# Performance work log

Hardware: AMD Instinct MI355X
Metric: run time of the kernel (lower is better)

## Reference

```python
import jax, jax.numpy as jnp
import numpy as np

B, LQ, LK, D, H, DK, DV = 8, 1024, 1024, 512, 8, 64, 64
EPS = 1e-14          # K.epsilon()**2 with default K.epsilon()=1e-7
MASK_VALUE = -1e30   # default mask_value in call()


def setup_inputs() -> dict:
    key = jax.random.key(0)
    ks = jax.random.split(key, 7)
    query = jax.random.normal(ks[0], (B, LQ, D), jnp.float32)
    key_t = jax.random.normal(ks[1], (B, LK, D), jnp.float32)
    value = jax.random.normal(ks[2], (B, LK, D), jnp.float32)
    mask = jax.random.randint(ks[3], (B, LK), 0, 2).astype(jnp.float32)
    glorot = np.sqrt(2.0 / (D + DK)).astype(np.float32)
    Wq = jax.random.normal(ks[4], (H, D, DK), jnp.float32) * glorot
    Wk = jax.random.normal(ks[5], (H, D, DK), jnp.float32) * glorot
    Wv = jax.random.normal(ks[6], (H, D, DV), jnp.float32) * glorot
    gamma = jnp.ones((1,), jnp.float32)
    beta = jnp.zeros((1,), jnp.float32)
    return {"query": query, "key": key_t, "value": value, "mask": mask,
            "Wq": Wq, "Wk": Wk, "Wv": Wv, "gamma": gamma, "beta": beta}


def reference(query, key, value, mask, Wq, Wk, Wv, gamma, beta):
    # Per-head projections (the original's Python loop over heads, vectorized).
    q = jnp.einsum('bqd,hde->bhqe', query, Wq)   # [B,H,LQ,DK]
    k = jnp.einsum('bkd,hde->bhke', key, Wk)     # [B,H,LK,DK]
    v = jnp.einsum('bkd,hde->bhke', value, Wv)   # [B,H,LK,DV]
    # NOTE: no 1/sqrt(dk) scaling, faithful to the source.
    A = jnp.einsum('bhqe,bhke->bhqk', q, k)      # [B,H,LQ,LK]
    m = mask[:, None, None, :]                    # [B,1,1,LK] broadcast over heads & queries
    A = m * A + (1.0 - m) * MASK_VALUE
    A = jax.nn.softmax(A, axis=-1)
    o = jnp.einsum('bhqk,bhke->bhqe', A, v)      # [B,H,LQ,DV]
    conc = o.transpose(0, 2, 1, 3).reshape(B, LQ, H * DV)  # concat heads
    # Scalar-affine layernorm over the concatenated feature dim.
    mean = jnp.mean(conc, axis=-1, keepdims=True)
    var = jnp.mean(jnp.square(conc - mean), axis=-1, keepdims=True)
    x = (conc - mean) / jnp.sqrt(var + EPS)
    return x * gamma[0] + beta[0]
```

## Files before the change

### kernel.cpp

```cpp
#include <hip/hip_runtime.h>
#include <math.h>

#define NB 8
#define NLQ 1024
#define NLK 1024
#define ND 512
#define NH 8
#define MASKV -1e30f
#define LOG2E 1.44269504088896f
#define SHIFT2 32.0f

typedef unsigned short ushort_t;
typedef __attribute__((ext_vector_type(8))) _Float16 f16x8;
typedef __attribute__((ext_vector_type(8))) short bf16x8;
typedef __attribute__((ext_vector_type(16))) float f32x16;

__device__ __forceinline__ ushort_t f2h_bits(float f) {
    union { _Float16 h; ushort_t u; } v; v.h = (_Float16)f;
    return v.u;
}
__device__ __forceinline__ ushort_t f2bf(float f) {
    union { float f; unsigned u; } v; v.f = f;
    unsigned r = v.u + 0x7fffu + ((v.u >> 16) & 1u);
    return (ushort_t)(r >> 16);
}
__device__ __forceinline__ void gload16(const ushort_t* g, ushort_t* l) {
    __builtin_amdgcn_global_load_lds(
        (const __attribute__((address_space(1))) void*)g,
        (__attribute__((address_space(3))) void*)l, 16, 0, 0);
}
__device__ __forceinline__ unsigned pack_bf16_trunc(float p0, float p1) {
    return __builtin_amdgcn_perm(__float_as_uint(p1), __float_as_uint(p0),
                                 0x07060302u);
}
__device__ __forceinline__ unsigned pack_f16(float a, float b) {
    return (unsigned)f2h_bits(a) | ((unsigned)f2h_bits(b) << 16);
}
__device__ __forceinline__ unsigned pack_bf16_rne(float a, float b) {
    return (unsigned)f2bf(a) | ((unsigned)f2bf(b) << 16);
}

__global__ __launch_bounds__(256) void wsplit_kernel(
    const float* __restrict__ Wq, const float* __restrict__ Wk, const float* __restrict__ Wv,
    ushort_t* __restrict__ oq, ushort_t* __restrict__ ok, ushort_t* __restrict__ ov) {
    __shared__ float T[64][65];
    const int d0 = blockIdx.x * 64;
    const int h  = blockIdx.y;
    const int t  = blockIdx.z;
    const float* W = (t == 0) ? Wq : (t == 1) ? Wk : Wv;
    ushort_t* oh = (t == 0) ? oq : (t == 1) ? ok : ov;
    const float scale = (t == 0) ? LOG2E : 1.f;
    const int tid = threadIdx.x;
#pragma unroll
    for (int i = 0; i < 4; i++) {
        int r = (tid >> 4) + i * 16;
        int c = (tid & 15) * 4;
        float4 v = *(const float4*)&W[((size_t)h * ND + d0 + r) * 64 + c];
        *(float4*)&T[r][c] = v;
    }
    __syncthreads();
    const int e = tid & 63;
    const int dg = tid >> 6;
    ushort_t hs[16];
#pragma unroll
    for (int dd = 0; dd < 16; dd++) hs[dd] = f2h_bits(T[dg * 16 + dd][e] * scale);
    size_t base = ((size_t)h * 64 + e) * ND + d0 + dg * 16;
#pragma unroll
    for (int c = 0; c < 2; c++) {
        uint4 wh;
        wh.x = (unsigned)hs[8*c+0] | ((unsigned)hs[8*c+1] << 16);
        wh.y = (unsigned)hs[8*c+2] | ((unsigned)hs[8*c+3] << 16);
        wh.z = (unsigned)hs[8*c+4] | ((unsigned)hs[8*c+5] << 16);
        wh.w = (unsigned)hs[8*c+6] | ((unsigned)hs[8*c+7] << 16);
        *(uint4*)&oh[base + 8 * c] = wh;
    }
}

__global__ __launch_bounds__(256, 3) void proj_mfma_kernel(
    const float* __restrict__ Xq, const float* __restrict__ Xk,
    const float* __restrict__ Xv, const ushort_t* __restrict__ Wbase,
    ushort_t* __restrict__ Obase) {
    __shared__ ushort_t sX[2][16 * 520];
    __shared__ ushort_t sW[2][8 * 520];

    const int lb = blockIdx.x * 128;
    const int h  = blockIdx.y;
    const int z  = blockIdx.z;
    const int t  = z >> 3;
    const int b  = z & 7;
    const int tid  = threadIdx.x;
    const int wave = tid >> 6;
    const int lane = tid & 63;
    const int l31  = lane & 31;
    const int hib  = lane >> 5;
    const int lhalf = wave & 1;
    const int ehalf = wave >> 1;
    const size_t bh = (size_t)b * NH + h;

    const float* Xt = (t == 0) ? Xq : (t == 1) ? Xk : Xv;
    const float* gx = Xt + ((size_t)b * NLQ + lb) * ND;
    const ushort_t* gw = Wbase + (size_t)t * ((size_t)NH * 64 * ND)
                       + (size_t)h * 64 * ND;
    ushort_t* out = Obase + (size_t)t * ((size_t)NB * NH * NLQ * 64);

    const int srow = lane >> 3;
    const int schk = (lane & 7) ^ srow;
    const int dslot = srow * 64 + (lane & 7) * 8;

    auto stage_w = [&](int buf, int d0) {
#pragma unroll
        for (int i = 0; i < 2; i++) {
            int u = i * 4 + wave;
            int row = u * 8 + srow;
            gload16(gw + (size_t)row * ND + d0 + schk * 8, sW[buf] + u * 520);
        }
    };
    auto load_x = [&](int d0, float4* xa, float4* xb) {
#pragma unroll
        for (int i = 0; i < 4; i++) {
            int u = i * 4 + wave;
            int row = u * 8 + srow;
            const float* src = gx + (size_t)row * ND + d0 + schk * 8;
            xa[i] = *(const float4*)src;
            xb[i] = *(const float4*)(src + 4);
        }
    };
    auto write_x = [&](int buf, const float4* xa, const float4* xb) {
#pragma unroll
        for (int i = 0; i < 4; i++) {
            int u = i * 4 + wave;
            uint4 w;
            w.x = pack_f16(xa[i].x, xa[i].y);
            w.y = pack_f16(xa[i].z, xa[i].w);
            w.z = pack_f16(xb[i].x, xb[i].y);
            w.w = pack_f16(xb[i].z, xb[i].w);
            *(uint4*)&sX[buf][u * 520 + dslot] = w;
        }
    };

    f32x16 acc0, acc1;
#pragma unroll
    for (int i = 0; i < 16; i++) { acc0[i] = 0.f; acc1[i] = 0.f; }

    const int arow0 = lhalf * 64 + l31;
    const int apad0 = (arow0 >> 3) * 520 + (arow0 & 7) * 64;
    const int apad1 = apad0 + 4 * 520;
    const int brow  = ehalf * 32 + l31;
    const int bpad  = (brow >> 3) * 520 + (brow & 7) * 64;
    const int sw = l31 & 7;

    {
        float4 xa[4], xb[4];
        load_x(0, xa, xb);
        stage_w(0, 0);
        write_x(0, xa, xb);
    }
    __syncthreads();
    int cur = 0;
    for (int kc = 0; kc < 8; kc++) {
        float4 xa[4], xb[4];
        if (kc < 7) {
            load_x((kc + 1) * 64, xa, xb);
            stage_w(cur ^ 1, (kc + 1) * 64);
        }
#pragma unroll
        for (int c = 0; c < 4; c++) {
            const int pc = ((2 * c + hib) ^ sw) * 8;
            f16x8 a0 = *(const f16x8*)&sX[cur][apad0 + pc];
            f16x8 a1 = *(const f16x8*)&sX[cur][apad1 + pc];
            f16x8 wv = *(const f16x8*)&sW[cur][bpad + pc];
            acc0 = __builtin_amdgcn_mfma_f32_32x32x16_f16(a0, wv, acc0, 0, 0, 0);
            acc1 = __builtin_amdgcn_mfma_f32_32x32x16_f16(a1, wv, acc1, 0, 0, 0);
        }
        if (kc < 7) write_x(cur ^ 1, xa, xb);
        __syncthreads();
        cur ^= 1;
    }

    if (t < 2) {
        const size_t ob = (bh * NLQ + lb + lhalf * 64) * 64;
        const int e = ehalf * 32 + l31;
#pragma unroll
        for (int r = 0; r < 16; r++) {
            int lr = (r & 3) + 8 * (r >> 2) + 4 * hib;
            out[ob + (size_t)lr * 64 + e]        = f2h_bits(acc0[r]);
            out[ob + (size_t)(32 + lr) * 64 + e] = f2h_bits(acc1[r]);
        }
    } else {
        ushort_t (*T)[136] = (ushort_t(*)[136])sX;
        const int e = ehalf * 32 + l31;
#pragma unroll
        for (int g = 0; g < 4; g++) {
            int lr = lhalf * 64 + 8 * g + 4 * hib;
            uint2 w0, w1;
            w0.x = pack_bf16_rne(acc0[4 * g + 0], acc0[4 * g + 1]);
            w0.y = pack_bf16_rne(acc0[4 * g + 2], acc0[4 * g + 3]);
            w1.x = pack_bf16_rne(acc1[4 * g + 0], acc1[4 * g + 1]);
            w1.y = pack_bf16_rne(acc1[4 * g + 2], acc1[4 * g + 3]);
            *(uint2*)&T[e][lr]      = w0;
            *(uint2*)&T[e][lr + 32] = w1;
        }
        __syncthreads();
        const int e2 = tid >> 2;
        const int lc = (tid & 3) * 32;
        size_t basev = (bh * 64 + e2) * NLK + lb + lc;
#pragma unroll
        for (int c4 = 0; c4 < 4; c4++)
            *(uint4*)&out[basev + c4 * 8] = *(const uint4*)&T[e2][lc + c4 * 8];
    }
}

__global__ __launch_bounds__(256, 4) void attn_kernel(
    const ushort_t* __restrict__ Qf, const ushort_t* __restrict__ Kf,
    const ushort_t* __restrict__ Vt, const float* __restrict__ maskp,
    float* __restrict__ Op) {
    __shared__ ushort_t sK[2][4160];
    __shared__ ushort_t sV[2][4160];
    __shared__ float sBias[1024];

    const int idx = blockIdx.x;
    const int bh_i = idx & 63;
    const int qc  = idx >> 6;
    const int b = bh_i >> 3, h = bh_i & 7;
    const size_t bh = (size_t)b * NH + h;

    const int tid  = threadIdx.x;
    const int wave = tid >> 6;
    const int lane = tid & 63;
    const int l31  = lane & 31;
    const int hib  = lane >> 5;
    const int q = qc * 128 + wave * 32 + l31;
    const int sw = l31 & 7;

    {
        const float* mrow = maskp + ((size_t)b << 10);
        float4 m0 = *(const float4*)&mrow[tid * 4];
        float4 bi;
        bi.x = (m0.x > 0.5f) ? -SHIFT2 : MASKV;
        bi.y = (m0.y > 0.5f) ? -SHIFT2 : MASKV;
        bi.z = (m0.z > 0.5f) ? -SHIFT2 : MASKV;
        bi.w = (m0.w > 0.5f) ? -SHIFT2 : MASKV;
        *(float4*)&sBias[tid * 4] = bi;
    }

    f16x8 qh[4];
    {
        const ushort_t* ph = Qf + (bh * NLQ + q) * 64 + hib * 8;
#pragma unroll
        for (int c = 0; c < 4; c++) qh[c] = *(const f16x8*)(ph + c * 16);
    }

    const int srow = lane >> 3;
    const int schk = (lane & 7) ^ srow;

    auto stage = [&](int buf, int k0) {
#pragma unroll
        for (int n = 0; n < 4; n++) {
            int u = wave + n * 4;
            if (u < 8) {
                int row = u * 8 + srow;
                int key = (row & ~12) | ((row & 4) << 1) | ((row & 8) >> 1);
                gload16(Kf + ((bh << 10) + k0 + key) * 64 + schk * 8,
                        sK[buf] + u * 520);
            } else {
                int u8 = u - 8;
                int row = u8 * 8 + srow;
                gload16(Vt + ((bh << 6) + row) * NLK + k0 + schk * 8,
                        sV[buf] + u8 * 520);
            }
        }
    };

    f32x16 O0, O1;
#pragma unroll
    for (int i = 0; i < 16; i++) { O0[i] = 0.f; O1[i] = 0.f; }
    float lrun = 0.f;

    const int rp0 = (l31 >> 3) * 520 + (l31 & 7) * 64;
    const int rp1 = rp0 + 4 * 520;

    stage(0, 0);
    __syncthreads();
    int cur = 0;

    for (int t = 0; t < 16; t++) {
        const int k0 = t << 6;
        if (t < 15) stage(cur ^ 1, k0 + 64);

        f32x16 S0, S1;
#pragma unroll
        for (int g = 0; g < 4; g++) {
            const int kb = k0 + 16 * (g >> 1) + 8 * hib + 4 * (g & 1);
            float4 b0 = *(const float4*)&sBias[kb];
            float4 b1 = *(const float4*)&sBias[kb + 32];
            S0[4 * g + 0] = b0.x; S0[4 * g + 1] = b0.y;
            S0[4 * g + 2] = b0.z; S0[4 * g + 3] = b0.w;
            S1[4 * g + 0] = b1.x; S1[4 * g + 1] = b1.y;
            S1[4 * g + 2] = b1.z; S1[4 * g + 3] = b1.w;
        }
#pragma unroll
        for (int c = 0; c < 4; c++) {
            const int pc = ((2 * c + hib) ^ sw) * 8;
            f16x8 a0 = *(const f16x8*)&sK[cur][rp0 + pc];
            f16x8 a1 = *(const f16x8*)&sK[cur][rp1 + pc];
            S0 = __builtin_amdgcn_mfma_f32_32x32x16_f16(a0, qh[c], S0, 0, 0, 0);
            S1 = __builtin_amdgcn_mfma_f32_32x32x16_f16(a1, qh[c], S1, 0, 0, 0);
        }

        unsigned pq[8][2];
#pragma unroll
        for (int g = 0; g < 8; g++) {
            float p0, p1, p2, p3;
            if (g < 4) {
                p0 = __builtin_amdgcn_exp2f(S0[4*g+0]);
                p1 = __builtin_amdgcn_exp2f(S0[4*g+1]);
                p2 = __builtin_amdgcn_exp2f(S0[4*g+2]);
                p3 = __builtin_amdgcn_exp2f(S0[4*g+3]);
            } else {
                p0 = __builtin_amdgcn_exp2f(S1[4*(g-4)+0]);
                p1 = __builtin_amdgcn_exp2f(S1[4*(g-4)+1]);
                p2 = __builtin_amdgcn_exp2f(S1[4*(g-4)+2]);
                p3 = __builtin_amdgcn_exp2f(S1[4*(g-4)+3]);
            }
            lrun += (p0 + p1) + (p2 + p3);
            pq[g][0] = pack_bf16_trunc(p0, p1);
            pq[g][1] = pack_bf16_trunc(p2, p3);
        }

#pragma unroll
        for (int c = 0; c < 4; c++) {
            union { unsigned u[4]; bf16x8 v; } pf;
            pf.u[0] = pq[2 * c][0];     pf.u[1] = pq[2 * c][1];
            pf.u[2] = pq[2 * c + 1][0]; pf.u[3] = pq[2 * c + 1][1];
            const int pc = ((2 * c + hib) ^ sw) * 8;
            bf16x8 v0 = *(const bf16x8*)&sV[cur][rp0 + pc];
            bf16x8 v1 = *(const bf16x8*)&sV[cur][rp1 + pc];
            O0 = __builtin_amdgcn_mfma_f32_32x32x16_bf16(v0, pf.v, O0, 0, 0, 0);
            O1 = __builtin_amdgcn_mfma_f32_32x32x16_bf16(v1, pf.v, O1, 0, 0, 0);
        }
        __syncthreads();
        cur ^= 1;
    }

    lrun += __shfl_xor(lrun, 32);
    const float linv = 1.f / lrun;
    float* obase = Op + ((size_t)(b * NLQ + q)) * (NH * 64) + h * 64;
#pragma unroll
    for (int me = 0; me < 2; me++) {
#pragma unroll
        for (int g = 0; g < 4; g++) {
            int e0 = me * 32 + 8 * g + 4 * hib;
            float4 o;
            if (me == 0) {
                o.x = O0[4 * g + 0] * linv; o.y = O0[4 * g + 1] * linv;
                o.z = O0[4 * g + 2] * linv; o.w = O0[4 * g + 3] * linv;
            } else {
                o.x = O1[4 * g + 0] * linv; o.y = O1[4 * g + 1] * linv;
                o.z = O1[4 * g + 2] * linv; o.w = O1[4 * g + 3] * linv;
            }
            *(float4*)&obase[e0] = o;
        }
    }
}

__global__ __launch_bounds__(256) void ln_kernel(const float* __restrict__ X,
                                                 const float* __restrict__ gamma,
                                                 const float* __restrict__ beta,
                                                 float* __restrict__ out) {
    const int row = blockIdx.x * 4 + (threadIdx.x >> 6);
    const int lane = threadIdx.x & 63;
    const float* x = &X[(size_t)row * 512];
    float4 v0 = *(const float4*)&x[lane * 8];
    float4 v1 = *(const float4*)&x[lane * 8 + 4];
    float sum = v0.x + v0.y + v0.z + v0.w + v1.x + v1.y + v1.z + v1.w;
    float sq = v0.x * v0.x + v0.y * v0.y + v0.z * v0.z + v0.w * v0.w
             + v1.x * v1.x + v1.y * v1.y + v1.z * v1.z + v1.w * v1.w;
#pragma unroll
    for (int off = 32; off > 0; off >>= 1) {
        sum += __shfl_down(sum, off);
        sq  += __shfl_down(sq, off);
    }
    sum = __shfl(sum, 0);
    sq  = __shfl(sq, 0);
    const float mean = sum * (1.f / 512.f);
    const float var = sq * (1.f / 512.f) - mean * mean;
    const float rstd = rsqrtf(var + 1e-14f);
    const float g = gamma[0], be = beta[0];
    float* o = &out[(size_t)row * 512];
    float4 r0, r1;
    r0.x = (v0.x - mean) * rstd * g + be;  r0.y = (v0.y - mean) * rstd * g + be;
    r0.z = (v0.z - mean) * rstd * g + be;  r0.w = (v0.w - mean) * rstd * g + be;
    r1.x = (v1.x - mean) * rstd * g + be;  r1.y = (v1.y - mean) * rstd * g + be;
    r1.z = (v1.z - mean) * rstd * g + be;  r1.w = (v1.w - mean) * rstd * g + be;
    *(float4*)&o[lane * 8] = r0;
    *(float4*)&o[lane * 8 + 4] = r1;
}

extern "C" void kernel_launch(void* const* d_in, const int* in_sizes, int n_in,
                              void* d_out, int out_size, void* d_ws, size_t ws_size,
                              hipStream_t stream) {
    const float* query = (const float*)d_in[0];
    const float* key_t = (const float*)d_in[1];
    const float* value = (const float*)d_in[2];
    const float* mask  = (const float*)d_in[3];
    const float* Wq    = (const float*)d_in[4];
    const float* Wk    = (const float*)d_in[5];
    const float* Wv    = (const float*)d_in[6];
    const float* gamma = (const float*)d_in[7];
    const float* beta  = (const float*)d_in[8];
    float* out = (float*)d_out;

    const size_t A = (size_t)NB * NLQ * ND;
    const size_t WS = (size_t)NH * 64 * ND;
    ushort_t* Qf = (ushort_t*)d_ws;
    ushort_t* Kf = Qf + A;
    ushort_t* Vt = Qf + 2 * A;
    ushort_t* Wt = Qf + 3 * A;

    wsplit_kernel<<<dim3(ND / 64, NH, 3), 256, 0, stream>>>(
        Wq, Wk, Wv, Wt, Wt + WS, Wt + 2 * WS);

    proj_mfma_kernel<<<dim3(NLQ / 128, NH, 24), 256, 0, stream>>>(
        query, key_t, value, Wt, Qf);

    attn_kernel<<<512, 256, 0, stream>>>(Qf, Kf, Vt, mask, out);

    ln_kernel<<<(NB * NLQ) / 4, 256, 0, stream>>>(out, gamma, beta, out);
}
```

Before: 171.1 us.

## Restructure projection kernel: full weight tile resident, per-wave 64-row X pipelines

```diff
diff --git a/kernel.cpp b/kernel.cpp
--- a/kernel.cpp
+++ b/kernel.cpp
@@ -76,14 +76,14 @@
     }
 }
 
-__global__ __launch_bounds__(256, 3) void proj_mfma_kernel(
+__global__ __launch_bounds__(256) void proj_mfma_kernel(
     const float* __restrict__ Xq, const float* __restrict__ Xk,
     const float* __restrict__ Xv, const ushort_t* __restrict__ Wbase,
     ushort_t* __restrict__ Obase) {
-    __shared__ ushort_t sX[2][16 * 520];
-    __shared__ ushort_t sW[2][8 * 520];
-
-    const int lb = blockIdx.x * 128;
+    __shared__ ushort_t sW[8][4160];
+    __shared__ ushort_t sX[4][2][4160];
+
+    const int lb = blockIdx.x * 256;
     const int h  = blockIdx.y;
     const int z  = blockIdx.z;
     const int t  = z >> 3;
@@ -93,12 +93,10 @@
     const int lane = tid & 63;
     const int l31  = lane & 31;
     const int hib  = lane >> 5;
-    const int lhalf = wave & 1;
-    const int ehalf = wave >> 1;
     const size_t bh = (size_t)b * NH + h;
 
     const float* Xt = (t == 0) ? Xq : (t == 1) ? Xk : Xv;
-    const float* gx = Xt + ((size_t)b * NLQ + lb) * ND;
+    const float* gx = Xt + ((size_t)b * NLQ + lb + wave * 64) * ND;
     const ushort_t* gw = Wbase + (size_t)t * ((size_t)NH * 64 * ND)
                        + (size_t)h * 64 * ND;
     ushort_t* out = Obase + (size_t)t * ((size_t)NB * NH * NLQ * 64);
@@ -107,106 +105,116 @@
     const int schk = (lane & 7) ^ srow;
     const int dslot = srow * 64 + (lane & 7) * 8;
 
-    auto stage_w = [&](int buf, int d0) {
+#pragma unroll
+    for (int kc = 0; kc < 8; kc++) {
 #pragma unroll
         for (int i = 0; i < 2; i++) {
             int u = i * 4 + wave;
             int row = u * 8 + srow;
-            gload16(gw + (size_t)row * ND + d0 + schk * 8, sW[buf] + u * 520);
-        }
-    };
-    auto load_x = [&](int d0, float4* xa, float4* xb) {
-#pragma unroll
-        for (int i = 0; i < 4; i++) {
-            int u = i * 4 + wave;
-            int row = u * 8 + srow;
-            const float* src = gx + (size_t)row * ND + d0 + schk * 8;
-            xa[i] = *(const float4*)src;
-            xb[i] = *(const float4*)(src + 4);
-        }
-    };
-    auto write_x = [&](int buf, const float4* xa, const float4* xb) {
-#pragma unroll
-        for (int i = 0; i < 4; i++) {
-            int u = i * 4 + wave;
-            uint4 w;
-            w.x = pack_f16(xa[i].x, xa[i].y);
-            w.y = pack_f16(xa[i].z, xa[i].w);
-            w.z = pack_f16(xb[i].x, xb[i].y);
-            w.w = pack_f16(xb[i].z, xb[i].w);
-            *(uint4*)&sX[buf][u * 520 + dslot] = w;
-        }
-    };
-
-    f32x16 acc0, acc1;
-#pragma unroll
-    for (int i = 0; i < 16; i++) { acc0[i] = 0.f; acc1[i] = 0.f; }
-
-    const int arow0 = lhalf * 64 + l31;
-    const int apad0 = (arow0 >> 3) * 520 + (arow0 & 7) * 64;
+            gload16(gw + (size_t)row * ND + kc * 64 + schk * 8,
+                    sW[kc] + u * 520);
+        }
+    }
+    float4 xa[8], xb[8];
+#pragma unroll
+    for (int g = 0; g < 8; g++) {
+        const float* src = gx + (size_t)(g * 8 + srow) * ND + schk * 8;
+        xa[g] = *(const float4*)src;
+        xb[g] = *(const float4*)(src + 4);
+    }
+    __syncthreads();
+#pragma unroll
+    for (int g = 0; g < 8; g++) {
+        uint4 w;
+        w.x = pack_f16(xa[g].x, xa[g].y);
+        w.y = pack_f16(xa[g].z, xa[g].w);
+        w.z = pack_f16(xb[g].x, xb[g].y);
+        w.w = pack_f16(xb[g].z, xb[g].w);
+        *(uint4*)&sX[wave][0][g * 520 + dslot] = w;
+    }
+
+    f32x16 a00, a01, a10, a11;
+#pragma unroll
+    for (int i = 0; i < 16; i++) { a00[i] = 0.f; a01[i] = 0.f; a10[i] = 0.f; a11[i] = 0.f; }
+
+    const int sw = l31 & 7;
+    const int apad0 = (l31 >> 3) * 520 + (l31 & 7) * 64;
     const int apad1 = apad0 + 4 * 520;
-    const int brow  = ehalf * 32 + l31;
-    const int bpad  = (brow >> 3) * 520 + (brow & 7) * 64;
-    const int sw = l31 & 7;
-
-    {
-        float4 xa[4], xb[4];
-        load_x(0, xa, xb);
-        stage_w(0, 0);
-        write_x(0, xa, xb);
-    }
-    __syncthreads();
+    const int bpad0 = apad0;
+    const int bpad1 = apad1;
+
     int cur = 0;
+#pragma unroll
     for (int kc = 0; kc < 8; kc++) {
-        float4 xa[4], xb[4];
+        float4 ya[8], yb[8];
         if (kc < 7) {
-            load_x((kc + 1) * 64, xa, xb);
-            stage_w(cur ^ 1, (kc + 1) * 64);
+            const float* gsrc = gx + (kc + 1) * 64;
+#pragma unroll
+            for (int g = 0; g < 8; g++) {
+                const float* src = gsrc + (size_t)(g * 8 + srow) * ND + schk * 8;
+                ya[g] = *(const float4*)src;
+                yb[g] = *(const float4*)(src + 4);
+            }
         }
 #pragma unroll
         for (int c = 0; c < 4; c++) {
             const int pc = ((2 * c + hib) ^ sw) * 8;
-            f16x8 a0 = *(const f16x8*)&sX[cur][apad0 + pc];
-            f16x8 a1 = *(const f16x8*)&sX[cur][apad1 + pc];
-            f16x8 wv = *(const f16x8*)&sW[cur][bpad + pc];
-            acc0 = __builtin_amdgcn_mfma_f32_32x32x16_f16(a0, wv, acc0, 0, 0, 0);
-            acc1 = __builtin_amdgcn_mfma_f32_32x32x16_f16(a1, wv, acc1, 0, 0, 0);
-        }
-        if (kc < 7) write_x(cur ^ 1, xa, xb);
-        __syncthreads();
+            f16x8 xv0 = *(const f16x8*)&sX[wave][cur][apad0 + pc];
+            f16x8 xv1 = *(const f16x8*)&sX[wave][cur][apad1 + pc];
+            f16x8 wv0 = *(const f16x8*)&sW[kc][bpad0 + pc];
+            f16x8 wv1 = *(const f16x8*)&sW[kc][bpad1 + pc];
+            a00 = __builtin_amdgcn_mfma_f32_32x32x16_f16(xv0, wv0, a00, 0, 0, 0);
+            a01 = __builtin_amdgcn_mfma_f32_32x32x16_f16(xv0, wv1, a01, 0, 0, 0);
+            a10 = __builtin_amdgcn_mfma_f32_32x32x16_f16(xv1, wv0, a10, 0, 0, 0);
+            a11 = __builtin_amdgcn_mfma_f32_32x32x16_f16(xv1, wv1, a11, 0, 0, 0);
+        }
+        if (kc < 7) {
+#pragma unroll
+            for (int g = 0; g < 8; g++) {
+                uint4 w;
+                w.x = pack_f16(ya[g].x, ya[g].y);
+                w.y = pack_f16(ya[g].z, ya[g].w);
+                w.z = pack_f16(yb[g].x, yb[g].y);
+                w.w = pack_f16(yb[g].z, yb[g].w);
+                *(uint4*)&sX[wave][cur ^ 1][g * 520 + dslot] = w;
+            }
+        }
         cur ^= 1;
     }
 
+    const int lbw = lb + wave * 64;
     if (t < 2) {
-        const size_t ob = (bh * NLQ + lb + lhalf * 64) * 64;
-        const int e = ehalf * 32 + l31;
+        const size_t ob = (bh * NLQ + lbw) * 64;
 #pragma unroll
         for (int r = 0; r < 16; r++) {
             int lr = (r & 3) + 8 * (r >> 2) + 4 * hib;
-            out[ob + (size_t)lr * 64 + e]        = f2h_bits(acc0[r]);
-            out[ob + (size_t)(32 + lr) * 64 + e] = f2h_bits(acc1[r]);
+            out[ob + (size_t)lr * 64 + l31]             = f2h_bits(a00[r]);
+            out[ob + (size_t)lr * 64 + 32 + l31]        = f2h_bits(a01[r]);
+            out[ob + (size_t)(32 + lr) * 64 + l31]      = f2h_bits(a10[r]);
+            out[ob + (size_t)(32 + lr) * 64 + 32 + l31] = f2h_bits(a11[r]);
         }
     } else {
-        ushort_t (*T)[136] = (ushort_t(*)[136])sX;
-        const int e = ehalf * 32 + l31;
+        ushort_t (*T)[68] = (ushort_t(*)[68])sX[wave];
 #pragma unroll
         for (int g = 0; g < 4; g++) {
-            int lr = lhalf * 64 + 8 * g + 4 * hib;
-            uint2 w0, w1;
-            w0.x = pack_bf16_rne(acc0[4 * g + 0], acc0[4 * g + 1]);
-            w0.y = pack_bf16_rne(acc0[4 * g + 2], acc0[4 * g + 3]);
-            w1.x = pack_bf16_rne(acc1[4 * g + 0], acc1[4 * g + 1]);
-            w1.y = pack_bf16_rne(acc1[4 * g + 2], acc1[4 * g + 3]);
-            *(uint2*)&T[e][lr]      = w0;
-            *(uint2*)&T[e][lr + 32] = w1;
-        }
-        __syncthreads();
-        const int e2 = tid >> 2;
-        const int lc = (tid & 3) * 32;
-        size_t basev = (bh * 64 + e2) * NLK + lb + lc;
-#pragma unroll
-        for (int c4 = 0; c4 < 4; c4++)
-            *(uint4*)&out[basev + c4 * 8] = *(const uint4*)&T[e2][lc + c4 * 8];
+            int lq4 = 8 * g + 4 * hib;
+            *(uint2*)&T[l31][lq4] = make_uint2(
+                pack_bf16_rne(a00[4 * g + 0], a00[4 * g + 1]),
+                pack_bf16_rne(a00[4 * g + 2], a00[4 * g + 3]));
+            *(uint2*)&T[32 + l31][lq4] = make_uint2(
+                pack_bf16_rne(a01[4 * g + 0], a01[4 * g + 1]),
+                pack_bf16_rne(a01[4 * g + 2], a01[4 * g + 3]));
+            *(uint2*)&T[l31][32 + lq4] = make_uint2(
+                pack_bf16_rne(a10[4 * g + 0], a10[4 * g + 1]),
+                pack_bf16_rne(a10[4 * g + 2], a10[4 * g + 3]));
+            *(uint2*)&T[32 + l31][32 + lq4] = make_uint2(
+                pack_bf16_rne(a11[4 * g + 0], a11[4 * g + 1]),
+                pack_bf16_rne(a11[4 * g + 2], a11[4 * g + 3]));
+        }
+        size_t basev = (bh * 64 + lane) * NLK + lbw;
+#pragma unroll
+        for (int c4 = 0; c4 < 8; c4++)
+            *(uint4*)&out[basev + c4 * 8] = *(const uint4*)&T[lane][c4 * 8];
     }
 }
 
@@ -420,7 +428,7 @@
     wsplit_kernel<<<dim3(ND / 64, NH, 3), 256, 0, stream>>>(
         Wq, Wk, Wv, Wt, Wt + WS, Wt + 2 * WS);
 
-    proj_mfma_kernel<<<dim3(NLQ / 128, NH, 24), 256, 0, stream>>>(
+    proj_mfma_kernel<<<dim3(4, NH, 24), 256, 0, stream>>>(
         query, key_t, value, Wt, Qf);
 
     attn_kernel<<<512, 256, 0, stream>>>(Qf, Kf, Vt, mask, out);
```

New measurement: 189.0 us. 1.1x slower.
